# Optimization experiments

Measured on AMD Instinct MI355X. Metric: run time of the kernel, lower is better.

## Reference

```python
import jax, jax.numpy as jnp
import numpy as np

NS = 100000  # senders
NR = 100000  # receivers
E = 600000   # edges
D = 128      # sender_dim = receiver_dim = edge_dim
EPS = 1e-5


def _layer_norm(x, g, b):
    mu = jnp.mean(x, axis=-1, keepdims=True)
    var = jnp.mean(jnp.square(x - mu), axis=-1, keepdims=True)
    return (x - mu) * jax.lax.rsqrt(var + EPS) * g + b


def _gcast_mlp(x, W, b, gamma, beta):
    # Faithful to GCastMLP.forward: z = silu(linear(x)); z = LN(silu(z))
    z = jax.nn.silu(x @ W.T + b)
    return _layer_norm(jax.nn.silu(z), gamma, beta)


def setup_inputs() -> dict:
    key = jax.random.key(0)
    ks = jax.random.split(key, 12)
    s = 1.0 / np.sqrt(3 * D)
    inp = {
        "sender_x": jax.random.normal(ks[0], (NS, D), jnp.float32),
        "receiver_x": jax.random.normal(ks[1], (NR, D), jnp.float32),
        "edge_index": jax.random.randint(ks[2], (2, E), 0, NR, jnp.int32),
        "edge_attr": jax.random.normal(ks[3], (E, D), jnp.float32),
        # edge MLP: in = sender+receiver+edge = 3D, out = edge_dim
        "We": jax.random.uniform(ks[4], (D, 3 * D), jnp.float32, -s, s),
        "be": jnp.zeros((D,), jnp.float32),
        "ge": jnp.ones((D,), jnp.float32),
        "bbe": jnp.zeros((D,), jnp.float32),
        # node MLP: in = receiver+edge = 2D, out = receiver_dim
        "Wn": jax.random.uniform(ks[5], (D, 2 * D), jnp.float32, -1.0 / np.sqrt(2 * D), 1.0 / np.sqrt(2 * D)),
        "bn": jnp.zeros((D,), jnp.float32),
        "gn": jnp.ones((D,), jnp.float32),
        "bbn": jnp.zeros((D,), jnp.float32),
        # sender MLP: square D -> D
        "Ws": jax.random.uniform(ks[6], (D, D), jnp.float32, -1.0 / np.sqrt(D), 1.0 / np.sqrt(D)),
        "bs": jnp.zeros((D,), jnp.float32),
        "gs": jnp.ones((D,), jnp.float32),
        "bbs": jnp.zeros((D,), jnp.float32),
    }
    return inp


def reference(sender_x, receiver_x, edge_index, edge_attr,
              We, be, ge, bbe, Wn, bn, gn, bbn, Ws, bs, gs, bbs):
    src, dst = edge_index[0], edge_index[1]
    # Edge encoder: gather endpoints, concat, MLP -> new edge features [E, D]
    edge_in = jnp.concatenate([sender_x[src], receiver_x[dst], edge_attr], axis=-1)
    edge_attr_p = _gcast_mlp(edge_in, We, be, ge, bbe)
    # Node encoder: scatter-sum messages (= new edge features) to receivers
    edge_aggr = jax.ops.segment_sum(edge_attr_p, dst, num_segments=receiver_x.shape[0])
    mesh_x_p = _gcast_mlp(jnp.concatenate([receiver_x, edge_aggr], axis=-1), Wn, bn, gn, bbn)
    # Residual updates
    sender_out = sender_x + _gcast_mlp(sender_x, Ws, bs, gs, bbs)
    receiver_out = receiver_x + mesh_x_p
    edge_out = edge_attr + edge_attr_p
    return (sender_out, receiver_out, edge_out)
```

## Files before the change

### kernel.cpp

```cpp
#include <hip/hip_runtime.h>
#include <stdint.h>


typedef __bf16 bf16x8 __attribute__((ext_vector_type(8)));
typedef float  f32x4  __attribute__((ext_vector_type(4)));

union U16B { uint4 u; bf16x8 v; };
union BFPK { __bf16 h[2]; unsigned int u; };
union BF1  { __bf16 h; unsigned short s; };

__device__ __forceinline__ float silu_f(float x) {
  return x * __builtin_amdgcn_rcpf(1.0f + __expf(-x));
}
__device__ __forceinline__ float bfu2f(unsigned int lo16) {
  return __uint_as_float(lo16 << 16);
}
__device__ __forceinline__ bf16x8 cvt8(float4 a, float4 b) {
  bf16x8 r;
  r[0] = (__bf16)a.x; r[1] = (__bf16)a.y; r[2] = (__bf16)a.z; r[3] = (__bf16)a.w;
  r[4] = (__bf16)b.x; r[5] = (__bf16)b.y; r[6] = (__bf16)b.z; r[7] = (__bf16)b.w;
  return r;
}

__global__ void prep_kernel(const float* __restrict__ We,
                            const float* __restrict__ Wn,
                            const float* __restrict__ Ws,
                            unsigned short* __restrict__ wimg,
                            const float* __restrict__ sx,
                            unsigned short* __restrict__ sb,
                            const float* __restrict__ rx,
                            unsigned short* __restrict__ rb,
                            int n8s, int n8r) {
  int i = blockIdx.x * 256 + threadIdx.x;
  if (i < 6 * 16384) {
    int panel = i >> 14;
    int r = (i >> 7) & 127;
    int csw = i & 127;
    int c_or = ((csw * 2) ^ ((r & 15) << 4)) >> 1;
    float f;
    if (panel < 3)      f = We[r * 384 + panel * 128 + c_or];
    else if (panel < 5) f = Wn[r * 256 + (panel - 3) * 128 + c_or];
    else                f = Ws[r * 128 + c_or];
    BF1 c; c.h = (__bf16)f;
    wimg[i] = c.s;
    return;
  }
  int j = i - 6 * 16384;
  const float* in; unsigned short* out; int idx;
  if (j < n8s) { in = sx; out = sb; idx = j; }
  else if (j < n8s + n8r) { in = rx; out = rb; idx = j - n8s; }
  else return;
  float4 a = reinterpret_cast<const float4*>(in)[2 * idx];
  float4 b = reinterpret_cast<const float4*>(in)[2 * idx + 1];
  U16B r8; r8.v = cvt8(a, b);
  reinterpret_cast<uint4*>(out)[idx] = r8.u;
}

__global__ void hist_kernel(const int* __restrict__ dst, int* __restrict__ counts, int E) {
  int i = blockIdx.x * 256 + threadIdx.x;
  if (i < E) atomicAdd(&counts[dst[i]], 1);
}

__global__ void scan1_kernel(const int* __restrict__ counts, int* __restrict__ pre,
                             int* __restrict__ blockSums, int n) {
  __shared__ int sh[256];
  const int t = threadIdx.x;
  const int base = blockIdx.x * 1024 + t * 4;
  int c0 = (base + 0 < n) ? counts[base + 0] : 0;
  int c1 = (base + 1 < n) ? counts[base + 1] : 0;
  int c2 = (base + 2 < n) ? counts[base + 2] : 0;
  int c3 = (base + 3 < n) ? counts[base + 3] : 0;
  int tot = c0 + c1 + c2 + c3;
  sh[t] = tot;
  __syncthreads();
  #pragma unroll
  for (int off = 1; off < 256; off <<= 1) {
    int v = (t >= off) ? sh[t - off] : 0;
    __syncthreads();
    sh[t] += v;
    __syncthreads();
  }
  int excl = sh[t] - tot;
  if (base + 0 < n) pre[base + 0] = excl;
  if (base + 1 < n) pre[base + 1] = excl + c0;
  if (base + 2 < n) pre[base + 2] = excl + c0 + c1;
  if (base + 3 < n) pre[base + 3] = excl + c0 + c1 + c2;
  if (t == 255) blockSums[blockIdx.x] = sh[255];
}

__global__ void scan2_kernel(int* __restrict__ blockSums, int nb) {
  __shared__ int sh[512];
  const int t = threadIdx.x;
  int v = (t < nb) ? blockSums[t] : 0;
  sh[t] = v;
  __syncthreads();
  #pragma unroll
  for (int off = 1; off < 512; off <<= 1) {
    int u = (t >= off) ? sh[t - off] : 0;
    __syncthreads();
    sh[t] += u;
    __syncthreads();
  }
  if (t < nb) blockSums[t] = sh[t] - v;
}

__global__ void scan3_kernel(const int* __restrict__ pre, const int* __restrict__ blockSums,
                             int* __restrict__ offs, int* __restrict__ cursor, int n) {
  int i = blockIdx.x * 256 + threadIdx.x;
  if (i >= n) return;
  int o = pre[i] + blockSums[i >> 10];
  offs[i] = o;
  cursor[i] = o;
}

__global__ void scatter_kernel(const int* __restrict__ dst, int* __restrict__ cursor,
                               int* __restrict__ rank, int E) {
  int i = blockIdx.x * 256 + threadIdx.x;
  if (i < E) {
    int p = atomicAdd(&cursor[dst[i]], 1);
    rank[i] = p;
  }
}

__global__ __launch_bounds__(256) void agg_kernel(
    const unsigned short* __restrict__ P,
    const int* __restrict__ offs, const int* __restrict__ counts,
    unsigned short* __restrict__ aggr, int NR) {
  const int l = threadIdx.x & 31;
  const int g0 = (blockIdx.x * 256 + threadIdx.x) >> 5;
  if (g0 >= NR) return;
  int beg = offs[g0];
  int cnt = counts[g0];
  float s0 = 0.f, s1 = 0.f, s2 = 0.f, s3 = 0.f;
  const unsigned short* p = P + (size_t)beg * 128 + l * 4;
  for (int k = 0; k < cnt; ++k) {
    uint2 w = *reinterpret_cast<const uint2*>(p);
    p += 128;
    s0 += bfu2f(w.x & 0xffffu);
    s1 += bfu2f(w.x >> 16);
    s2 += bfu2f(w.y & 0xffffu);
    s3 += bfu2f(w.y >> 16);
  }
  BFPK a, b;
  a.h[0] = (__bf16)s0; a.h[1] = (__bf16)s1;
  b.h[0] = (__bf16)s2; b.h[1] = (__bf16)s3;
  uint2 o; o.x = a.u; o.y = b.u;
  *reinterpret_cast<uint2*>(aggr + (size_t)g0 * 128 + l * 4) = o;
}

template <int KDIM, int AGGR>
__global__ __launch_bounds__(512, 4) void mlp_v9_kernel(
    const unsigned short* __restrict__ s0, const int* __restrict__ i0,
    const unsigned short* __restrict__ s1, const int* __restrict__ i1,
    const float* __restrict__ s2,
    const unsigned short* __restrict__ Wb,
    const float* __restrict__ bias, const float* __restrict__ gamma,
    const float* __restrict__ beta,
    const float* __restrict__ resid,
    float* __restrict__ outp,
    void* aggr, const int* __restrict__ aggr_idx,
    const int* __restrict__ prank,
    int M) {
  constexpr int NSEG = KDIM / 128;
  __shared__ __align__(16) unsigned short smem[2][16384];

  const int tid = threadIdx.x;
  const int wid = tid >> 6;
  const int lane = tid & 63;
  const int l15 = lane & 15;
  const int q = lane >> 4;
  const int l31 = lane & 31;
  const int rhalf = lane >> 5;
  const int wrow = blockIdx.x * 128 + wid * 16;
  const int xm = l15 << 3;

  int rr = wrow + l15;
  if (rr >= M) rr = M - 1;
  const unsigned short* p0 = s0 + (size_t)(i0 ? i0[rr] : rr) * 128;
  const unsigned short* p1 = nullptr;
  const float* p2 = nullptr;
  if constexpr (KDIM >= 256) p1 = s1 + (size_t)(i1 ? i1[rr] : rr) * 128;
  if constexpr (KDIM >= 384) p2 = s2 + (size_t)rr * 128;

  auto stageB = [&](int seg, int buf) {
    const unsigned short* g = Wb + seg * 16384 + wid * 2048 + lane * 8;
    unsigned short* l = &smem[buf][wid * 2048];
    #pragma unroll
    for (int u = 0; u < 4; ++u) {
      __builtin_amdgcn_global_load_lds(
          (const __attribute__((address_space(1))) unsigned int*)(g + u * 512),
          (__attribute__((address_space(3))) unsigned int*)(l + u * 512),
          16, 0, 0);
    }
  };

  stageB(0, 0);
  if constexpr (NSEG > 1) stageB(1, 1);

  U16B A0[4], A1[4];
  float4 A2r[8];
  #pragma unroll
  for (int k4 = 0; k4 < 4; ++k4) {
    A0[k4].u = *reinterpret_cast<const uint4*>(p0 + k4 * 32 + q * 8);
    if constexpr (KDIM >= 256)
      A1[k4].u = *reinterpret_cast<const uint4*>(p1 + k4 * 32 + q * 8);
    if constexpr (KDIM >= 384) {
      A2r[2 * k4]     = reinterpret_cast<const float4*>(p2 + k4 * 32 + q * 8)[0];
      A2r[2 * k4 + 1] = reinterpret_cast<const float4*>(p2 + k4 * 32 + q * 8)[1];
    }
  }
  __builtin_amdgcn_sched_barrier(0);
  __syncthreads();

  f32x4 acc[8] = {};

  auto mfmaSeg = [&](int buf, const U16B (&A)[4]) {
    #pragma unroll
    for (int k4 = 0; k4 < 4; ++k4) {
      #pragma unroll
      for (int n = 0; n < 8; ++n) {
        U16B b;
        b.u = *reinterpret_cast<const uint4*>(
            &smem[buf][(n * 16 + l15) * 128 + ((k4 * 32 + q * 8) ^ xm)]);
        acc[n] = __builtin_amdgcn_mfma_f32_16x16x32_bf16(A[k4].v, b.v, acc[n], 0, 0, 0);
      }
    }
  };

  mfmaSeg(0, A0);
  if constexpr (NSEG >= 2) {
    __syncthreads();
    if constexpr (NSEG >= 3) stageB(2, 0);
    mfmaSeg(1, A1);
    if constexpr (NSEG >= 3) {
      __syncthreads();
      U16B A2[4];
      #pragma unroll
      for (int k4 = 0; k4 < 4; ++k4) A2[k4].v = cvt8(A2r[2 * k4], A2r[2 * k4 + 1]);
      mfmaSeg(0, A2);
    }
  }

  unsigned short* yw = (NSEG == 2 ? &smem[0][0] : &smem[1][0]) + wid * (16 * 132);

  float bia[8];
  #pragma unroll
  for (int n = 0; n < 8; ++n) bia[n] = bias[n * 16 + l15];

  float sum[4] = {0.f, 0.f, 0.f, 0.f};
  float ssq[4] = {0.f, 0.f, 0.f, 0.f};
  #pragma unroll
  for (int n = 0; n < 8; ++n) {
    #pragma unroll
    for (int j = 0; j < 4; ++j) {
      float t = silu_f(silu_f(acc[n][j] + bia[n]));
      acc[n][j] = t;
      sum[j] += t;
      ssq[j] += t * t;
    }
  }
  #pragma unroll
  for (int off = 1; off < 16; off <<= 1) {
    #pragma unroll
    for (int j = 0; j < 4; ++j) {
      sum[j] += __shfl_xor(sum[j], off);
      ssq[j] += __shfl_xor(ssq[j], off);
    }
  }
  float mu[4], rs[4];
  #pragma unroll
  for (int j = 0; j < 4; ++j) {
    mu[j] = sum[j] * (1.0f / 128.0f);
    float var = ssq[j] * (1.0f / 128.0f) - mu[j] * mu[j];
    rs[j] = rsqrtf(var + 1e-5f);
  }
  float gam[8], bet[8];
  #pragma unroll
  for (int n = 0; n < 8; ++n) {
    gam[n] = gamma[n * 16 + l15];
    bet[n] = beta[n * 16 + l15];
  }

  #pragma unroll
  for (int n = 0; n < 8; ++n) {
    #pragma unroll
    for (int j = 0; j < 4; ++j) {
      float y = (acc[n][j] - mu[j]) * rs[j] * gam[n] + bet[n];
      BF1 c; c.h = (__bf16)y;
      yw[(q * 4 + j) * 132 + n * 16 + l15] = c.s;
    }
  }
  asm volatile("s_waitcnt lgkmcnt(0)" ::: "memory");

  #pragma unroll
  for (int s = 0; s < 8; ++s) {
    int row16 = 2 * s + rhalf;
    int grow = wrow + row16;
    uint2 w = *reinterpret_cast<const uint2*>(&yw[row16 * 132 + l31 * 4]);
    if (grow < M) {
      const f32x4 r4 = *reinterpret_cast<const f32x4*>(resid + (size_t)grow * 128 + l31 * 4);
      f32x4 o4;
      o4.x = r4.x + bfu2f(w.x & 0xffffu);
      o4.y = r4.y + bfu2f(w.x >> 16);
      o4.z = r4.z + bfu2f(w.y & 0xffffu);
      o4.w = r4.w + bfu2f(w.y >> 16);
      __builtin_nontemporal_store(o4, reinterpret_cast<f32x4*>(outp + (size_t)grow * 128 + l31 * 4));
      if constexpr (AGGR == 3) {
        int prow = prank[grow];
        *reinterpret_cast<uint2*>((unsigned short*)aggr + (size_t)prow * 128 + l31 * 4) = w;
      } else if constexpr (AGGR == 2) {
        int idx = aggr_idx[grow];
        unsigned short* ar = (unsigned short*)aggr + (size_t)idx * 128 + l31 * 4;
        asm volatile("global_atomic_pk_add_bf16 %0, %1, off" :: "v"(ar), "v"(w.x) : "memory");
        asm volatile("global_atomic_pk_add_bf16 %0, %1, off" :: "v"(ar + 2), "v"(w.y) : "memory");
      }
    }
  }
}

template <int KDIM>
__global__ __launch_bounds__(512, 4) void mlp_fb_kernel(
    const float* __restrict__ s0, const int* __restrict__ i0,
    const float* __restrict__ s1, const int* __restrict__ i1,
    const float* __restrict__ s2,
    const unsigned short* __restrict__ Wb,
    const float* __restrict__ bias, const float* __restrict__ gamma,
    const float* __restrict__ beta,
    const float* __restrict__ resid,
    float* __restrict__ outp,
    float* aggr, const int* __restrict__ aggr_idx,
    int M) {
  constexpr int NSEG = KDIM / 128;
  __shared__ __align__(16) unsigned short smem[2][16384];
  const int tid = threadIdx.x;
  const int wid = tid >> 6;
  const int lane = tid & 63;
  const int l15 = lane & 15;
  const int q = lane >> 4;
  const int l31 = lane & 31;
  const int rhalf = lane >> 5;
  const int wrow = blockIdx.x * 128 + wid * 16;
  const int xm = l15 << 3;

  int rr = wrow + l15;
  if (rr >= M) rr = M - 1;
  const float* p0 = s0 + (size_t)(i0 ? i0[rr] : rr) * 128;
  const float* p1 = (KDIM >= 256) ? (s1 + (size_t)(i1 ? i1[rr] : rr) * 128) : nullptr;
  const float* p2 = (KDIM >= 384) ? (s2 + (size_t)rr * 128) : nullptr;

  auto stageB = [&](int seg, int buf) {
    const unsigned short* g = Wb + seg * 16384 + wid * 2048 + lane * 8;
    unsigned short* l = &smem[buf][wid * 2048];
    #pragma unroll
    for (int u = 0; u < 4; ++u) {
      __builtin_amdgcn_global_load_lds(
          (const __attribute__((address_space(1))) unsigned int*)(g + u * 512),
          (__attribute__((address_space(3))) unsigned int*)(l + u * 512),
          16, 0, 0);
    }
  };

  stageB(0, 0);
  f32x4 acc[8] = {};
  __syncthreads();
  int cur = 0;
  #pragma unroll
  for (int seg = 0; seg < NSEG; ++seg) {
    if (seg + 1 < NSEG) stageB(seg + 1, cur ^ 1);
    const float* base = (seg == 0) ? p0 : ((seg == 1) ? p1 : p2);
    #pragma unroll
    for (int k4 = 0; k4 < 4; ++k4) {
      const float4* pp = reinterpret_cast<const float4*>(base + k4 * 32 + q * 8);
      U16B a; a.v = cvt8(pp[0], pp[1]);
      #pragma unroll
      for (int n = 0; n < 8; ++n) {
        U16B b;
        b.u = *reinterpret_cast<const uint4*>(
            &smem[cur][(n * 16 + l15) * 128 + ((k4 * 32 + q * 8) ^ xm)]);
        acc[n] = __builtin_amdgcn_mfma_f32_16x16x32_bf16(a.v, b.v, acc[n], 0, 0, 0);
      }
    }
    __syncthreads();
    if (seg + 1 < NSEG) cur ^= 1;
  }

  unsigned short* yw = &smem[0][0] + wid * (16 * 132);
  float bia[8];
  #pragma unroll
  for (int n = 0; n < 8; ++n) bia[n] = bias[n * 16 + l15];
  float sum[4] = {0.f, 0.f, 0.f, 0.f}, ssq[4] = {0.f, 0.f, 0.f, 0.f};
  #pragma unroll
  for (int n = 0; n < 8; ++n)
    #pragma unroll
    for (int j = 0; j < 4; ++j) {
      float t = silu_f(silu_f(acc[n][j] + bia[n]));
      acc[n][j] = t; sum[j] += t; ssq[j] += t * t;
    }
  #pragma unroll
  for (int off = 1; off < 16; off <<= 1)
    #pragma unroll
    for (int j = 0; j < 4; ++j) {
      sum[j] += __shfl_xor(sum[j], off);
      ssq[j] += __shfl_xor(ssq[j], off);
    }
  float mu[4], rs[4];
  #pragma unroll
  for (int j = 0; j < 4; ++j) {
    mu[j] = sum[j] * (1.0f / 128.0f);
    float var = ssq[j] * (1.0f / 128.0f) - mu[j] * mu[j];
    rs[j] = rsqrtf(var + 1e-5f);
  }
  float gam[8], bet[8];
  #pragma unroll
  for (int n = 0; n < 8; ++n) { gam[n] = gamma[n * 16 + l15]; bet[n] = beta[n * 16 + l15]; }
  #pragma unroll
  for (int n = 0; n < 8; ++n)
    #pragma unroll
    for (int j = 0; j < 4; ++j) {
      float y = (acc[n][j] - mu[j]) * rs[j] * gam[n] + bet[n];
      BF1 c; c.h = (__bf16)y;
      yw[(q * 4 + j) * 132 + n * 16 + l15] = c.s;
    }
  asm volatile("s_waitcnt lgkmcnt(0)" ::: "memory");
  #pragma unroll
  for (int s = 0; s < 8; ++s) {
    int row16 = 2 * s + rhalf;
    int grow = wrow + row16;
    uint2 w = *reinterpret_cast<const uint2*>(&yw[row16 * 132 + l31 * 4]);
    if (grow < M) {
      const f32x4 r4 = *reinterpret_cast<const f32x4*>(resid + (size_t)grow * 128 + l31 * 4);
      f32x4 o4;
      o4.x = r4.x + bfu2f(w.x & 0xffffu);
      o4.y = r4.y + bfu2f(w.x >> 16);
      o4.z = r4.z + bfu2f(w.y & 0xffffu);
      o4.w = r4.w + bfu2f(w.y >> 16);
      __builtin_nontemporal_store(o4, reinterpret_cast<f32x4*>(outp + (size_t)grow * 128 + l31 * 4));
      if (aggr) {
        int idx = aggr_idx[grow];
        float* ar = aggr + (size_t)idx * 128 + l31 * 4;
        atomicAdd(ar + 0, bfu2f(w.x & 0xffffu));
        atomicAdd(ar + 1, bfu2f(w.x >> 16));
        atomicAdd(ar + 2, bfu2f(w.y & 0xffffu));
        atomicAdd(ar + 3, bfu2f(w.y >> 16));
      }
    }
  }
}

extern "C" void kernel_launch(void* const* d_in, const int* in_sizes, int n_in,
                              void* d_out, int out_size, void* d_ws, size_t ws_size,
                              hipStream_t stream) {
  const float* sender_x   = (const float*)d_in[0];
  const float* receiver_x = (const float*)d_in[1];
  const int*   edge_index = (const int*)d_in[2];
  const float* edge_attr  = (const float*)d_in[3];
  const float* We  = (const float*)d_in[4];
  const float* be  = (const float*)d_in[5];
  const float* ge  = (const float*)d_in[6];
  const float* bbe = (const float*)d_in[7];
  const float* Wn  = (const float*)d_in[8];
  const float* bn  = (const float*)d_in[9];
  const float* gn  = (const float*)d_in[10];
  const float* bbn = (const float*)d_in[11];
  const float* Ws  = (const float*)d_in[12];
  const float* bs  = (const float*)d_in[13];
  const float* gs  = (const float*)d_in[14];
  const float* bbs = (const float*)d_in[15];

  const int D  = 128;
  const int NS = in_sizes[0] / D;
  const int NR = in_sizes[1] / D;
  const int E  = in_sizes[2] / 2;

  const int* src = edge_index;
  const int* dst = edge_index + E;

  float* out          = (float*)d_out;
  float* sender_out   = out;
  float* receiver_out = out + (size_t)NS * D;
  float* edge_out     = out + (size_t)(NS + NR) * D;

  const size_t welems = 6 * 16384;
  unsigned short* We_b = (unsigned short*)d_ws;
  unsigned short* Wn_b = We_b + 3 * 16384;
  unsigned short* Ws_b = We_b + 5 * 16384;
  unsigned short* sender_b   = We_b + welems;
  unsigned short* receiver_b = sender_b + (size_t)NS * D;
  unsigned short* aggr_b     = receiver_b + (size_t)NR * D;
  unsigned short* P_b        = aggr_b + (size_t)NR * D;
  int* counts    = (int*)(P_b + (size_t)E * D);
  int* pre       = counts + NR;
  int* offs      = pre + NR;
  int* cursor    = offs + NR;
  int* blockSums = cursor + NR;
  int* rank      = blockSums + 512;

  const int nScanBlocks = (NR + 1023) / 1024;
  const size_t needCSR = 2 * (welems + (size_t)(NS + 2 * NR) * D + (size_t)E * D)
                       + 4 * (4 * (size_t)NR + 512 + (size_t)E);
  const size_t needA = (welems + (size_t)(NS + 2 * NR) * D) * 2;

  int tier;
  if (ws_size >= needCSR && nScanBlocks <= 512) tier = 0;
  else if (ws_size >= needA) tier = 1;
  else tier = 2;

  const int gridE = (E + 127) / 128;
  const int gridR = (NR + 127) / 128;
  const int gridS = (NS + 127) / 128;
  const int n8s = NS * D / 8, n8r = NR * D / 8;

  if (tier <= 1) {
    const int prepItems = (int)welems + n8s + n8r;
    prep_kernel<<<(prepItems + 255) / 256, 256, 0, stream>>>(
        We, Wn, Ws, We_b, sender_x, sender_b, receiver_x, receiver_b, n8s, n8r);
  } else {
    prep_kernel<<<(int)((welems + 255) / 256), 256, 0, stream>>>(
        We, Wn, Ws, We_b, nullptr, nullptr, nullptr, nullptr, 0, 0);
  }

  if (tier == 0) {
    (void)hipMemsetAsync(counts, 0, (size_t)NR * 4, stream);
    hist_kernel<<<(E + 255) / 256, 256, 0, stream>>>(dst, counts, E);
    scan1_kernel<<<nScanBlocks, 256, 0, stream>>>(counts, pre, blockSums, NR);
    scan2_kernel<<<1, 512, 0, stream>>>(blockSums, nScanBlocks);
    scan3_kernel<<<(NR + 255) / 256, 256, 0, stream>>>(pre, blockSums, offs, cursor, NR);
    scatter_kernel<<<(E + 255) / 256, 256, 0, stream>>>(dst, cursor, rank, E);

    mlp_v9_kernel<384, 3><<<gridE, 512, 0, stream>>>(
        sender_b, src, receiver_b, dst, edge_attr,
        We_b, be, ge, bbe, edge_attr, edge_out, P_b, nullptr, rank, E);

    agg_kernel<<<(NR + 7) / 8, 256, 0, stream>>>(P_b, offs, counts, aggr_b, NR);

    mlp_v9_kernel<256, 0><<<gridR, 512, 0, stream>>>(
        receiver_b, nullptr, aggr_b, nullptr, nullptr,
        Wn_b, bn, gn, bbn, receiver_x, receiver_out, nullptr, nullptr, nullptr, NR);

    mlp_v9_kernel<128, 0><<<gridS, 512, 0, stream>>>(
        sender_b, nullptr, nullptr, nullptr, nullptr,
        Ws_b, bs, gs, bbs, sender_x, sender_out, nullptr, nullptr, nullptr, NS);
  } else if (tier == 1) {
    (void)hipMemsetAsync(aggr_b, 0, (size_t)NR * D * 2, stream);

    mlp_v9_kernel<384, 2><<<gridE, 512, 0, stream>>>(
        sender_b, src, receiver_b, dst, edge_attr,
        We_b, be, ge, bbe, edge_attr, edge_out, aggr_b, dst, nullptr, E);

    mlp_v9_kernel<256, 0><<<gridR, 512, 0, stream>>>(
        receiver_b, nullptr, aggr_b, nullptr, nullptr,
        Wn_b, bn, gn, bbn, receiver_x, receiver_out, nullptr, nullptr, nullptr, NR);

    mlp_v9_kernel<128, 0><<<gridS, 512, 0, stream>>>(
        sender_b, nullptr, nullptr, nullptr, nullptr,
        Ws_b, bs, gs, bbs, sender_x, sender_out, nullptr, nullptr, nullptr, NS);
  } else {
    (void)hipMemsetAsync(receiver_out, 0, (size_t)NR * D * sizeof(float), stream);

    mlp_fb_kernel<384><<<gridE, 512, 0, stream>>>(
        sender_x, src, receiver_x, dst, edge_attr,
        We_b, be, ge, bbe, edge_attr, edge_out, receiver_out, dst, E);

    mlp_fb_kernel<256><<<gridR, 512, 0, stream>>>(
        receiver_x, nullptr, receiver_out, nullptr, nullptr,
        Wn_b, bn, gn, bbn, receiver_x, receiver_out, nullptr, nullptr, NR);

    mlp_fb_kernel<128><<<gridS, 512, 0, stream>>>(
        sender_x, nullptr, nullptr, nullptr, nullptr,
        Ws_b, bs, gs, bbs, sender_x, sender_out, nullptr, nullptr, NS);
  }
}
```

Measured before the change: 454.5 us.

## Single-buffer weight panels to raise MLP occupancy and fuse histogram into prep

The MLP kernel drops from a double-buffered 64KB LDS weight stage to a single 32KB buffer and raises launch bounds from 4 to 6 blocks. A loops over K segments, prefetching the next A fragment into registers while computing. The LN epilogue is split into two halves so the output staging fits the smaller buffer. The edge histogram is folded into the prep kernel to remove one launch. The cost is extra barriers and serialised weight staging between segments, so less of the weight load overlaps compute.

```diff
diff --git a/kernel.cpp b/kernel.cpp
--- a/kernel.cpp
+++ b/kernel.cpp
@@ -30,7 +30,9 @@
                             unsigned short* __restrict__ sb,
                             const float* __restrict__ rx,
                             unsigned short* __restrict__ rb,
-                            int n8s, int n8r) {
+                            int n8s, int n8r,
+                            const int* __restrict__ dst,
+                            int* __restrict__ counts, int E) {
   int i = blockIdx.x * 256 + threadIdx.x;
   if (i < 6 * 16384) {
     int panel = i >> 14;
@@ -46,19 +48,18 @@
     return;
   }
   int j = i - 6 * 16384;
-  const float* in; unsigned short* out; int idx;
-  if (j < n8s) { in = sx; out = sb; idx = j; }
-  else if (j < n8s + n8r) { in = rx; out = rb; idx = j - n8s; }
-  else return;
-  float4 a = reinterpret_cast<const float4*>(in)[2 * idx];
-  float4 b = reinterpret_cast<const float4*>(in)[2 * idx + 1];
-  U16B r8; r8.v = cvt8(a, b);
-  reinterpret_cast<uint4*>(out)[idx] = r8.u;
-}
-
-__global__ void hist_kernel(const int* __restrict__ dst, int* __restrict__ counts, int E) {
-  int i = blockIdx.x * 256 + threadIdx.x;
-  if (i < E) atomicAdd(&counts[dst[i]], 1);
+  if (j < n8s + n8r) {
+    const float* in; unsigned short* out; int idx;
+    if (j < n8s) { in = sx; out = sb; idx = j; }
+    else         { in = rx; out = rb; idx = j - n8s; }
+    float4 a = reinterpret_cast<const float4*>(in)[2 * idx];
+    float4 b = reinterpret_cast<const float4*>(in)[2 * idx + 1];
+    U16B r8; r8.v = cvt8(a, b);
+    reinterpret_cast<uint4*>(out)[idx] = r8.u;
+    return;
+  }
+  int e = j - n8s - n8r;
+  if (e < E) atomicAdd(&counts[dst[e]], 1);
 }
 
 __global__ void scan1_kernel(const int* __restrict__ counts, int* __restrict__ pre,
@@ -149,7 +150,7 @@
 }
 
 template <int KDIM, int AGGR>
-__global__ __launch_bounds__(512, 4) void mlp_v9_kernel(
+__global__ __launch_bounds__(512, 6) void mlp_v10_kernel(
     const unsigned short* __restrict__ s0, const int* __restrict__ i0,
     const unsigned short* __restrict__ s1, const int* __restrict__ i1,
     const float* __restrict__ s2,
@@ -162,7 +163,7 @@
     const int* __restrict__ prank,
     int M) {
   constexpr int NSEG = KDIM / 128;
-  __shared__ __align__(16) unsigned short smem[2][16384];
+  __shared__ __align__(16) unsigned short smem[16384];
 
   const int tid = threadIdx.x;
   const int wid = tid >> 6;
@@ -182,9 +183,9 @@
   if constexpr (KDIM >= 256) p1 = s1 + (size_t)(i1 ? i1[rr] : rr) * 128;
   if constexpr (KDIM >= 384) p2 = s2 + (size_t)rr * 128;
 
-  auto stageB = [&](int seg, int buf) {
+  auto stageB = [&](int seg) {
     const unsigned short* g = Wb + seg * 16384 + wid * 2048 + lane * 8;
-    unsigned short* l = &smem[buf][wid * 2048];
+    unsigned short* l = &smem[wid * 2048];
     #pragma unroll
     for (int u = 0; u < 4; ++u) {
       __builtin_amdgcn_global_load_lds(
@@ -194,54 +195,49 @@
     }
   };
 
-  stageB(0, 0);
-  if constexpr (NSEG > 1) stageB(1, 1);
-
-  U16B A0[4], A1[4];
-  float4 A2r[8];
-  #pragma unroll
-  for (int k4 = 0; k4 < 4; ++k4) {
-    A0[k4].u = *reinterpret_cast<const uint4*>(p0 + k4 * 32 + q * 8);
-    if constexpr (KDIM >= 256)
-      A1[k4].u = *reinterpret_cast<const uint4*>(p1 + k4 * 32 + q * 8);
-    if constexpr (KDIM >= 384) {
-      A2r[2 * k4]     = reinterpret_cast<const float4*>(p2 + k4 * 32 + q * 8)[0];
-      A2r[2 * k4 + 1] = reinterpret_cast<const float4*>(p2 + k4 * 32 + q * 8)[1];
-    }
-  }
-  __builtin_amdgcn_sched_barrier(0);
+  U16B Ac[4], An[4];
+  auto loadA = [&](int seg, U16B (&dst)[4]) {
+    #pragma unroll
+    for (int k4 = 0; k4 < 4; ++k4) {
+      const int kof = k4 * 32 + q * 8;
+      if (seg == 0) {
+        dst[k4].u = *reinterpret_cast<const uint4*>(p0 + kof);
+      } else if (seg == 1) {
+        dst[k4].u = *reinterpret_cast<const uint4*>(p1 + kof);
+      } else {
+        const float4* p = reinterpret_cast<const float4*>(p2 + kof);
+        dst[k4].v = cvt8(p[0], p[1]);
+      }
+    }
+  };
+
+  f32x4 acc[8] = {};
+
+  stageB(0);
+  loadA(0, Ac);
   __syncthreads();
 
-  f32x4 acc[8] = {};
-
-  auto mfmaSeg = [&](int buf, const U16B (&A)[4]) {
+  #pragma unroll
+  for (int seg = 0; seg < NSEG; ++seg) {
+    if (seg + 1 < NSEG) loadA(seg + 1, An);
     #pragma unroll
     for (int k4 = 0; k4 < 4; ++k4) {
       #pragma unroll
       for (int n = 0; n < 8; ++n) {
         U16B b;
         b.u = *reinterpret_cast<const uint4*>(
-            &smem[buf][(n * 16 + l15) * 128 + ((k4 * 32 + q * 8) ^ xm)]);
-        acc[n] = __builtin_amdgcn_mfma_f32_16x16x32_bf16(A[k4].v, b.v, acc[n], 0, 0, 0);
+            &smem[(n * 16 + l15) * 128 + ((k4 * 32 + q * 8) ^ xm)]);
+        acc[n] = __builtin_amdgcn_mfma_f32_16x16x32_bf16(Ac[k4].v, b.v, acc[n], 0, 0, 0);
       }
     }
-  };
-
-  mfmaSeg(0, A0);
-  if constexpr (NSEG >= 2) {
     __syncthreads();
-    if constexpr (NSEG >= 3) stageB(2, 0);
-    mfmaSeg(1, A1);
-    if constexpr (NSEG >= 3) {
+    if (seg + 1 < NSEG) {
+      stageB(seg + 1);
       __syncthreads();
-      U16B A2[4];
       #pragma unroll
-      for (int k4 = 0; k4 < 4; ++k4) A2[k4].v = cvt8(A2r[2 * k4], A2r[2 * k4 + 1]);
-      mfmaSeg(0, A2);
-    }
-  }
-
-  unsigned short* yw = (NSEG == 2 ? &smem[0][0] : &smem[1][0]) + wid * (16 * 132);
+      for (int k4 = 0; k4 < 4; ++k4) Ac[k4] = An[k4];
+    }
+  }
 
   float bia[8];
   #pragma unroll
@@ -281,38 +277,48 @@
     bet[n] = beta[n * 16 + l15];
   }
 
-  #pragma unroll
-  for (int n = 0; n < 8; ++n) {
-    #pragma unroll
-    for (int j = 0; j < 4; ++j) {
-      float y = (acc[n][j] - mu[j]) * rs[j] * gam[n] + bet[n];
-      BF1 c; c.h = (__bf16)y;
-      yw[(q * 4 + j) * 132 + n * 16 + l15] = c.s;
-    }
-  }
-  asm volatile("s_waitcnt lgkmcnt(0)" ::: "memory");
-
-  #pragma unroll
-  for (int s = 0; s < 8; ++s) {
-    int row16 = 2 * s + rhalf;
-    int grow = wrow + row16;
-    uint2 w = *reinterpret_cast<const uint2*>(&yw[row16 * 132 + l31 * 4]);
-    if (grow < M) {
-      const f32x4 r4 = *reinterpret_cast<const f32x4*>(resid + (size_t)grow * 128 + l31 * 4);
-      f32x4 o4;
-      o4.x = r4.x + bfu2f(w.x & 0xffffu);
-      o4.y = r4.y + bfu2f(w.x >> 16);
-      o4.z = r4.z + bfu2f(w.y & 0xffffu);
-      o4.w = r4.w + bfu2f(w.y >> 16);
-      __builtin_nontemporal_store(o4, reinterpret_cast<f32x4*>(outp + (size_t)grow * 128 + l31 * 4));
-      if constexpr (AGGR == 3) {
-        int prow = prank[grow];
-        *reinterpret_cast<uint2*>((unsigned short*)aggr + (size_t)prow * 128 + l31 * 4) = w;
-      } else if constexpr (AGGR == 2) {
-        int idx = aggr_idx[grow];
-        unsigned short* ar = (unsigned short*)aggr + (size_t)idx * 128 + l31 * 4;
-        asm volatile("global_atomic_pk_add_bf16 %0, %1, off" :: "v"(ar), "v"(w.x) : "memory");
-        asm volatile("global_atomic_pk_add_bf16 %0, %1, off" :: "v"(ar + 2), "v"(w.y) : "memory");
+  unsigned short* yw = &smem[wid * 2048];
+
+  #pragma unroll
+  for (int h = 0; h < 2; ++h) {
+    if (h == 1) {
+      asm volatile("s_waitcnt lgkmcnt(0)" ::: "memory");
+    }
+    if ((q >> 1) == h) {
+      #pragma unroll
+      for (int n = 0; n < 8; ++n) {
+        #pragma unroll
+        for (int j = 0; j < 4; ++j) {
+          float y = (acc[n][j] - mu[j]) * rs[j] * gam[n] + bet[n];
+          BF1 c; c.h = (__bf16)y;
+          yw[((q & 1) * 4 + j) * 132 + n * 16 + l15] = c.s;
+        }
+      }
+    }
+    asm volatile("s_waitcnt lgkmcnt(0)" ::: "memory");
+
+    #pragma unroll
+    for (int s = 0; s < 4; ++s) {
+      int row8 = 2 * s + rhalf;
+      int grow = wrow + 8 * h + row8;
+      uint2 w = *reinterpret_cast<const uint2*>(&yw[row8 * 132 + l31 * 4]);
+      if (grow < M) {
+        const f32x4 r4 = *reinterpret_cast<const f32x4*>(resid + (size_t)grow * 128 + l31 * 4);
+        f32x4 o4;
+        o4.x = r4.x + bfu2f(w.x & 0xffffu);
+        o4.y = r4.y + bfu2f(w.x >> 16);
+        o4.z = r4.z + bfu2f(w.y & 0xffffu);
+        o4.w = r4.w + bfu2f(w.y >> 16);
+        __builtin_nontemporal_store(o4, reinterpret_cast<f32x4*>(outp + (size_t)grow * 128 + l31 * 4));
+        if constexpr (AGGR == 3) {
+          int prow = prank[grow];
+          *reinterpret_cast<uint2*>((unsigned short*)aggr + (size_t)prow * 128 + l31 * 4) = w;
+        } else if constexpr (AGGR == 2) {
+          int idx = aggr_idx[grow];
+          unsigned short* ar = (unsigned short*)aggr + (size_t)idx * 128 + l31 * 4;
+          asm volatile("global_atomic_pk_add_bf16 %0, %1, off" :: "v"(ar), "v"(w.x) : "memory");
+          asm volatile("global_atomic_pk_add_bf16 %0, %1, off" :: "v"(ar + 2), "v"(w.y) : "memory");
+        }
       }
     }
   }
@@ -510,51 +516,53 @@
   const int gridS = (NS + 127) / 128;
   const int n8s = NS * D / 8, n8r = NR * D / 8;
 
-  if (tier <= 1) {
-    const int prepItems = (int)welems + n8s + n8r;
-    prep_kernel<<<(prepItems + 255) / 256, 256, 0, stream>>>(
-        We, Wn, Ws, We_b, sender_x, sender_b, receiver_x, receiver_b, n8s, n8r);
-  } else {
-    prep_kernel<<<(int)((welems + 255) / 256), 256, 0, stream>>>(
-        We, Wn, Ws, We_b, nullptr, nullptr, nullptr, nullptr, 0, 0);
-  }
-
   if (tier == 0) {
     (void)hipMemsetAsync(counts, 0, (size_t)NR * 4, stream);
-    hist_kernel<<<(E + 255) / 256, 256, 0, stream>>>(dst, counts, E);
+    const int prepItems = (int)welems + n8s + n8r + E;
+    prep_kernel<<<(prepItems + 255) / 256, 256, 0, stream>>>(
+        We, Wn, Ws, We_b, sender_x, sender_b, receiver_x, receiver_b,
+        n8s, n8r, dst, counts, E);
+
     scan1_kernel<<<nScanBlocks, 256, 0, stream>>>(counts, pre, blockSums, NR);
     scan2_kernel<<<1, 512, 0, stream>>>(blockSums, nScanBlocks);
     scan3_kernel<<<(NR + 255) / 256, 256, 0, stream>>>(pre, blockSums, offs, cursor, NR);
     scatter_kernel<<<(E + 255) / 256, 256, 0, stream>>>(dst, cursor, rank, E);
 
-    mlp_v9_kernel<384, 3><<<gridE, 512, 0, stream>>>(
+    mlp_v10_kernel<384, 3><<<gridE, 512, 0, stream>>>(
         sender_b, src, receiver_b, dst, edge_attr,
         We_b, be, ge, bbe, edge_attr, edge_out, P_b, nullptr, rank, E);
 
     agg_kernel<<<(NR + 7) / 8, 256, 0, stream>>>(P_b, offs, counts, aggr_b, NR);
 
-    mlp_v9_kernel<256, 0><<<gridR, 512, 0, stream>>>(
+    mlp_v10_kernel<256, 0><<<gridR, 512, 0, stream>>>(
         receiver_b, nullptr, aggr_b, nullptr, nullptr,
         Wn_b, bn, gn, bbn, receiver_x, receiver_out, nullptr, nullptr, nullptr, NR);
 
-    mlp_v9_kernel<128, 0><<<gridS, 512, 0, stream>>>(
+    mlp_v10_kernel<128, 0><<<gridS, 512, 0, stream>>>(
         sender_b, nullptr, nullptr, nullptr, nullptr,
         Ws_b, bs, gs, bbs, sender_x, sender_out, nullptr, nullptr, nullptr, NS);
   } else if (tier == 1) {
+    const int prepItems = (int)welems + n8s + n8r;
+    prep_kernel<<<(prepItems + 255) / 256, 256, 0, stream>>>(
+        We, Wn, Ws, We_b, sender_x, sender_b, receiver_x, receiver_b,
+        n8s, n8r, nullptr, nullptr, 0);
     (void)hipMemsetAsync(aggr_b, 0, (size_t)NR * D * 2, stream);
 
-    mlp_v9_kernel<384, 2><<<gridE, 512, 0, stream>>>(
+    mlp_v10_kernel<384, 2><<<gridE, 512, 0, stream>>>(
         sender_b, src, receiver_b, dst, edge_attr,
         We_b, be, ge, bbe, edge_attr, edge_out, aggr_b, dst, nullptr, E);
 
-    mlp_v9_kernel<256, 0><<<gridR, 512, 0, stream>>>(
+    mlp_v10_kernel<256, 0><<<gridR, 512, 0, stream>>>(
         receiver_b, nullptr, aggr_b, nullptr, nullptr,
         Wn_b, bn, gn, bbn, receiver_x, receiver_out, nullptr, nullptr, nullptr, NR);
 
-    mlp_v9_kernel<128, 0><<<gridS, 512, 0, stream>>>(
+    mlp_v10_kernel<128, 0><<<gridS, 512, 0, stream>>>(
         sender_b, nullptr, nullptr, nullptr, nullptr,
         Ws_b, bs, gs, bbs, sender_x, sender_out, nullptr, nullptr, nullptr, NS);
   } else {
+    prep_kernel<<<(int)((welems + 255) / 256), 256, 0, stream>>>(
+        We, Wn, Ws, We_b, nullptr, nullptr, nullptr, nullptr, 0, 0,
+        nullptr, nullptr, 0);
     (void)hipMemsetAsync(receiver_out, 0, (size_t)NR * D * sizeof(float), stream);
 
     mlp_fb_kernel<384><<<gridE, 512, 0, stream>>>(
```

New measurement: 450.0 us. No clear change (-1.0%).
